# Kernel optimization log

Measured on AMD Instinct MI355X. Metric: run time of the kernel, lower is better.

Reference implementation:

```python
import jax, jax.numpy as jnp
import numpy as np

EMBED_DIM = 1024
NUM_HEADS = 16
HEAD_DIM = EMBED_DIM // NUM_HEADS
ROPE_BASE = 10000.0
SQK_INIT_VALUE = 1.0
SQK_INIT_SCALING = 1.0 / (EMBED_DIM ** 0.5)


def setup_inputs() -> dict:
    key = jax.random.key(0)
    ks = jax.random.split(key, 6)
    B, N = 1, 2048
    x = jax.random.normal(ks[0], (B, N, EMBED_DIM), dtype=jnp.float32)
    # torch nn.Linear weights are [out_features, in_features]; y = x @ W.T
    s = EMBED_DIM ** -0.5
    Wq = jax.random.normal(ks[1], (EMBED_DIM, EMBED_DIM), dtype=jnp.float32) * s
    Wk = jax.random.normal(ks[2], (EMBED_DIM, EMBED_DIM), dtype=jnp.float32) * s
    Wv = jax.random.normal(ks[3], (EMBED_DIM, EMBED_DIM), dtype=jnp.float32) * s
    Wo = jax.random.normal(ks[4], (EMBED_DIM, EMBED_DIM), dtype=jnp.float32) * s
    sqk = SQK_INIT_SCALING * jnp.ones((EMBED_DIM,), dtype=jnp.float32) \
        + 0.01 * jax.random.normal(ks[5], (EMBED_DIM,), dtype=jnp.float32)
    return {"x": x, "Wq": Wq, "Wk": Wk, "Wv": Wv, "Wo": Wo, "sqk": sqk}


def _rope(t, offset=0):
    # t: [b, h, n, d]; rotary position embedding (Lrpe type 1), half-split layout
    d = t.shape[-1]
    n = t.shape[-2]
    inv_freq = 1.0 / (ROPE_BASE ** (jnp.arange(0, d, 2, dtype=jnp.float32) / d))  # [d/2]
    pos = jnp.arange(n, dtype=jnp.float32) + offset                               # [n]
    freqs = pos[:, None] * inv_freq[None, :]                                      # [n, d/2]
    cos = jnp.cos(freqs)
    sin = jnp.sin(freqs)
    t1, t2 = jnp.split(t, 2, axis=-1)
    return jnp.concatenate([t1 * cos - t2 * sin, t1 * sin + t2 * cos], axis=-1)


def _justnorm(t):
    return t / jnp.linalg.norm(t, axis=-1, keepdims=True)


def reference(x, Wq, Wk, Wv, Wo, sqk):
    B, N, E = x.shape
    H, D = NUM_HEADS, HEAD_DIM
    q = jnp.einsum('bne,fe->bnf', x, Wq).reshape(B, N, H, D).transpose(0, 2, 1, 3)
    k = jnp.einsum('bne,fe->bnf', x, Wk).reshape(B, N, H, D).transpose(0, 2, 1, 3)
    v = jnp.einsum('bne,fe->bnf', x, Wv).reshape(B, N, H, D).transpose(0, 2, 1, 3)
    q = _rope(q)
    k = _rope(k)
    # sqk * (init_value / init_scaling), reshaped to (h, 1, d)
    sqk_s = (sqk * (SQK_INIT_VALUE / SQK_INIT_SCALING)).reshape(H, 1, D)
    q = sqk_s * _justnorm(q)
    k = sqk_s * _justnorm(k)
    # SDPA with scale = sqrt(head_dim) (as in the source), causal
    scale = D ** 0.5
    scores = jnp.einsum('bhnd,bhmd->bhnm', q, k) * scale
    causal = jnp.tril(jnp.ones((N, N), dtype=bool))
    scores = jnp.where(causal, scores, -jnp.inf)
    attn = jax.nn.softmax(scores, axis=-1)
    out = jnp.einsum('bhnm,bhmd->bhnd', attn, v)           # [b,h,n,d]
    out = out.transpose(0, 2, 1, 3).reshape(B, N, E)       # [b,n,e]
    out = jnp.einsum('bne,fe->bnf', out, Wo)
    return out
```

## Files before the change

### kernel.cpp

```cpp
#include <hip/hip_runtime.h>
#include <hip/hip_bf16.h>

typedef float f32x4 __attribute__((ext_vector_type(4)));
typedef __bf16 bf16x8 __attribute__((ext_vector_type(8)));
typedef __bf16 bf16x4 __attribute__((ext_vector_type(4)));

__device__ __forceinline__ void gload_lds16(const __bf16* g, __bf16* l) {
  __builtin_amdgcn_global_load_lds(
      (const __attribute__((address_space(1))) void*)g,
      (__attribute__((address_space(3))) void*)l, 16, 0, 0);
}

__global__ __launch_bounds__(256) void convert_all(
    const float* __restrict__ x, const float* __restrict__ wq,
    const float* __restrict__ wk, const float* __restrict__ wv,
    const float* __restrict__ wo, __bf16* __restrict__ dst)
{
  int t = blockIdx.x * 256 + threadIdx.x;
  const float* src; size_t soff;
  if (t < 262144) { src = x; soff = (size_t)t * 8; }
  else {
    int r = (t - 262144) >> 17;
    src = (r == 0) ? wq : (r == 1) ? wk : (r == 2) ? wv : wo;
    soff = (size_t)((t - 262144) & 131071) * 8;
  }
  float4 f0 = *(const float4*)(src + soff);
  float4 f1 = *(const float4*)(src + soff + 4);
  bf16x8 o;
  o[0]=(__bf16)f0.x; o[1]=(__bf16)f0.y; o[2]=(__bf16)f0.z; o[3]=(__bf16)f0.w;
  o[4]=(__bf16)f1.x; o[5]=(__bf16)f1.y; o[6]=(__bf16)f1.z; o[7]=(__bf16)f1.w;
  *(bf16x8*)(dst + (size_t)t * 8) = o;
}

template <int BM, int BN, int BK, typename OutT, bool ROPE>
__global__ __launch_bounds__(256) void gemm_bt(
    const __bf16* __restrict__ A,
    const __bf16* __restrict__ B0, const __bf16* __restrict__ B1, const __bf16* __restrict__ B2,
    OutT* __restrict__ C0, OutT* __restrict__ C1, OutT* __restrict__ C2,
    int M, int N, int K, const float* __restrict__ sqkp)
{
  const __bf16* B = (blockIdx.z == 0) ? B0 : (blockIdx.z == 1) ? B1 : B2;
  OutT* C = (blockIdx.z == 0) ? C0 : (blockIdx.z == 1) ? C1 : C2;

  constexpr int MT = BM / 32, NT = BN / 32, KK = BK / 32;
  constexpr int CPR = BK / 8;
  constexpr int RPI = 64 / CPR;
  __shared__ __align__(16) __bf16 As[BM * BK];
  __shared__ __align__(16) __bf16 Bs[BN * BK];

  const int tid = threadIdx.x, w = tid >> 6, l = tid & 63;
  const int wr = w >> 1, wc = w & 1;
  const int g = l >> 4, c16 = l & 15;
  const int bm = blockIdx.y, bn = blockIdx.x;
  const int lr = l / CPR, lc = l % CPR;

  f32x4 acc[MT][NT] = {};
  const int nk = K / BK;

  for (int kt = 0; kt < nk; ++kt) {
    __syncthreads();
#pragma unroll
    for (int i = w; i < BM / RPI; i += 4) {
      int row = i * RPI + lr;
      int sch = lc ^ (row & 7);
      gload_lds16(A + (size_t)(bm * BM + row) * K + kt * BK + sch * 8, As + i * RPI * BK);
    }
#pragma unroll
    for (int i = w; i < BN / RPI; i += 4) {
      int row = i * RPI + lr;
      int sch = lc ^ (row & 7);
      gload_lds16(B + (size_t)(bn * BN + row) * K + kt * BK + sch * 8, Bs + i * RPI * BK);
    }
    __syncthreads();

#pragma unroll
    for (int kk = 0; kk < KK; ++kk) {
      bf16x8 af[MT], bf[NT];
#pragma unroll
      for (int mt = 0; mt < MT; ++mt) {
        int row = wr * (BM / 2) + mt * 16 + c16;
        af[mt] = *(const bf16x8*)(As + row * BK + (((kk * 4 + g) ^ (row & 7)) * 8));
      }
#pragma unroll
      for (int nt = 0; nt < NT; ++nt) {
        int row = wc * (BN / 2) + nt * 16 + c16;
        bf[nt] = *(const bf16x8*)(Bs + row * BK + (((kk * 4 + g) ^ (row & 7)) * 8));
      }
#pragma unroll
      for (int mt = 0; mt < MT; ++mt)
#pragma unroll
        for (int nt = 0; nt < NT; ++nt)
          acc[mt][nt] = __builtin_amdgcn_mfma_f32_16x16x32_bf16(af[mt], bf[nt], acc[mt][nt], 0, 0, 0);
    }
  }

  bool done = false;
  if constexpr (ROPE) {
    static_assert(!ROPE || NT == 4, "ROPE epilogue assumes BN=128");
    if (blockIdx.z < 2) {
      const bool isQ = (blockIdx.z == 0);
      const int hcol = bn * BN + wc * (BN / 2);
      float sq[4];
#pragma unroll
      for (int nt = 0; nt < 4; ++nt) sq[nt] = sqkp[hcol + nt * 16 + c16] * 32.0f;
      const float QSC = 8.0f * 1.4426950408889634f;
      const float L = 0.415241011860919f;
      const float inv0 = exp2f(-(float)c16 * L);
      const float inv1 = exp2f(-(float)(c16 + 16) * L);
#pragma unroll
      for (int mt = 0; mt < MT; ++mt) {
#pragma unroll
        for (int r = 0; r < 4; ++r) {
          int row = bm * BM + wr * (BM / 2) + mt * 16 + g * 4 + r;
          float s0, c0, s1, c1;
          sincosf((float)row * inv0, &s0, &c0);
          sincosf((float)row * inv1, &s1, &c1);
          float v0 = acc[mt][0][r], v1 = acc[mt][1][r];
          float v2 = acc[mt][2][r], v3 = acc[mt][3][r];
          float n0 = v0 * c0 - v2 * s0;
          float n2 = v0 * s0 + v2 * c0;
          float n1 = v1 * c1 - v3 * s1;
          float n3 = v1 * s1 + v3 * c1;
          float ss = n0 * n0 + n1 * n1 + n2 * n2 + n3 * n3;
#pragma unroll
          for (int m2 = 1; m2 < 16; m2 <<= 1) ss += __shfl_xor(ss, m2, 16);
          float rinv = rsqrtf(ss);
          if (isQ) rinv *= QSC;
          C[(size_t)row * N + hcol +  0 + c16] = (OutT)(n0 * sq[0] * rinv);
          C[(size_t)row * N + hcol + 16 + c16] = (OutT)(n1 * sq[1] * rinv);
          C[(size_t)row * N + hcol + 32 + c16] = (OutT)(n2 * sq[2] * rinv);
          C[(size_t)row * N + hcol + 48 + c16] = (OutT)(n3 * sq[3] * rinv);
        }
      }
      done = true;
    }
  }
  if (!done) {
#pragma unroll
    for (int mt = 0; mt < MT; ++mt)
#pragma unroll
      for (int nt = 0; nt < NT; ++nt)
#pragma unroll
        for (int r = 0; r < 4; ++r) {
          int row = bm * BM + wr * (BM / 2) + mt * 16 + g * 4 + r;
          int col = bn * BN + wc * (BN / 2) + nt * 16 + c16;
          C[(size_t)row * N + col] = (OutT)acc[mt][nt][r];
        }
  }
}

__global__ __launch_bounds__(256) void vtrans(const __bf16* __restrict__ v, __bf16* __restrict__ vt)
{
  __shared__ __align__(16) __bf16 t[64 * 72];
  int h = blockIdx.y;
  int n0 = blockIdx.x * 64;
  int tid = threadIdx.x;
#pragma unroll
  for (int j = 0; j < 2; ++j) {
    int idx = tid + j * 256;
    int r = idx >> 3, c = (idx & 7) * 8;
    bf16x8 val = *(const bf16x8*)(v + (size_t)(n0 + r) * 1024 + h * 64 + c);
    *(bf16x8*)&t[r * 72 + c] = val;
  }
  __syncthreads();
#pragma unroll
  for (int j = 0; j < 2; ++j) {
    int idx = tid + j * 256;
    int d = idx >> 3, nn = (idx & 7) * 8;
    bf16x8 o;
#pragma unroll
    for (int jj = 0; jj < 8; ++jj) o[jj] = t[(nn + jj) * 72 + d];
    *(bf16x8*)(vt + (size_t)(h * 64 + d) * 2048 + n0 + nn) = o;
  }
}

#define STAGE(BUF, KT)                                                         \
  {                                                                            \
    _Pragma("unroll")                                                          \
    for (int p = 0; p < 2; ++p) {                                              \
      int row = srow + p * 32;                                                 \
      int sch = sc ^ (row & 7);                                                \
      gload_lds16(Kg + (size_t)((KT) * 64 + row) * 1024 + h * 64 + sch * 8,    \
                  &Ks[BUF][w * 512 + p * 2048]);                               \
      gload_lds16(Vg + ((size_t)h * 64 + row) * 2048 + (KT) * 64 + sch * 8,    \
                  &Vs[BUF][w * 512 + p * 2048]);                               \
    }                                                                          \
  }

__global__ __launch_bounds__(256, 4) void attn_kernel(
    const __bf16* __restrict__ Qg, const __bf16* __restrict__ Kg,
    const __bf16* __restrict__ Vg, __bf16* __restrict__ Og,
    float* __restrict__ oS, float* __restrict__ lS)
{
  __shared__ __align__(16) __bf16 Ks[2][4096];
  __shared__ __align__(16) __bf16 Vs[2][4096];
  __shared__ __align__(16) __bf16 Ps[4][16 * 72];

  const int b = blockIdx.x;
  int h, qt, kts, kte, sidx;
  if (b < 512) {
    int p = b >> 5;
    qt = 16 + p;
    sidx = (b >> 4) & 1;
    h = b & 15;
    int mid = (qt + 1) >> 1;
    kts = sidx ? mid : 0;
    kte = sidx ? qt : (mid - 1);
  } else {
    qt = 15 - ((b - 512) >> 4);
    h = b & 15;
    kts = 0; kte = qt; sidx = -1;
  }
  const int q0 = qt * 64;

  const int tid = threadIdx.x, w = tid >> 6, l = tid & 63;
  const int g = l >> 4, c16 = l & 15;
  const int srow = tid >> 3;
  const int sc   = tid & 7;

  __bf16* Ps_w = &Ps[w][0];
  const int qig = q0 + w * 16 + c16;

  const __bf16* qbase = Qg + (size_t)qig * 1024 + h * 64 + g * 8;
  const bf16x8 qf0 = *(const bf16x8*)(qbase);
  const bf16x8 qf1 = *(const bf16x8*)(qbase + 32);

  f32x4 o[4] = {};
  float lsum = 0.f;

  STAGE(0, kts)

  for (int kt = kts; kt <= kte; ++kt) {
    const int cur = (kt - kts) & 1;
    __syncthreads();
    if (kt < kte) STAGE(cur ^ 1, kt + 1)

    const __bf16* Kb = Ks[cur];
    const __bf16* Vb = Vs[cur];

    f32x4 s[4] = {};
#pragma unroll
    for (int kjb = 0; kjb < 4; ++kjb) {
      int r = kjb * 16 + c16;
      bf16x8 k0 = *(const bf16x8*)((char*)Kb + r * 128 + ((g ^ (r & 7)) * 16));
      bf16x8 k1 = *(const bf16x8*)((char*)Kb + r * 128 + (((4 + g) ^ (r & 7)) * 16));
      s[kjb] = __builtin_amdgcn_mfma_f32_16x16x32_bf16(k0, qf0, s[kjb], 0, 0, 0);
      s[kjb] = __builtin_amdgcn_mfma_f32_16x16x32_bf16(k1, qf1, s[kjb], 0, 0, 0);
    }

    const bool diag = (kt == qt);
#pragma unroll
    for (int kjb = 0; kjb < 4; ++kjb) {
      bf16x4 pk;
#pragma unroll
      for (int r = 0; r < 4; ++r) {
        float sv = s[kjb][r];
        int kvg = kt * 64 + kjb * 16 + g * 4 + r;
        if (diag && kvg > qig) sv = -1e30f;
        float e = exp2f(sv);
        pk[r] = (__bf16)e;
        lsum += e;
      }
      *(bf16x4*)((char*)Ps_w + c16 * 144 + kjb * 32 + g * 8) = pk;
    }

#pragma unroll
    for (int ks = 0; ks < 2; ++ks) {
      bf16x8 pa = *(const bf16x8*)((char*)Ps_w + c16 * 144 + ks * 64 + g * 16);
#pragma unroll
      for (int nt = 0; nt < 4; ++nt) {
        int r = nt * 16 + c16;
        bf16x8 vb = *(const bf16x8*)((char*)Vb + r * 128 + (((ks * 4 + g) ^ (r & 7)) * 16));
        o[nt] = __builtin_amdgcn_mfma_f32_16x16x32_bf16(pa, vb, o[nt], 0, 0, 0);
      }
    }
  }

  lsum += __shfl_xor(lsum, 16);
  lsum += __shfl_xor(lsum, 32);

  if (sidx < 0) {
    float* lsh = (float*)Ps_w;
    if (g == 0) lsh[c16] = lsum;
    __builtin_amdgcn_s_waitcnt(0);
#pragma unroll
    for (int r = 0; r < 4; ++r) {
      float rinv = 1.0f / lsh[g * 4 + r];
      int qi = q0 + w * 16 + g * 4 + r;
#pragma unroll
      for (int nt = 0; nt < 4; ++nt)
        Og[(size_t)qi * 1024 + h * 64 + nt * 16 + c16] = (__bf16)(o[nt][r] * rinv);
    }
  } else {
    float* oBase = oS + (size_t)sidx * 1024 * 1024;
#pragma unroll
    for (int r = 0; r < 4; ++r) {
      int row = q0 + w * 16 + g * 4 + r - 1024;
#pragma unroll
      for (int nt = 0; nt < 4; ++nt)
        oBase[(size_t)row * 1024 + h * 64 + nt * 16 + c16] = o[nt][r];
    }
    if (g == 0)
      lS[(size_t)sidx * 1024 * 16 + (size_t)(qig - 1024) * 16 + h] = lsum;
  }
}

__global__ __launch_bounds__(256) void merge_halves(
    const float* __restrict__ oS, const float* __restrict__ lS,
    __bf16* __restrict__ Og)
{
  int row = blockIdx.x;
  int col = threadIdx.x * 4;
  int h = col >> 6;
  float lsum = lS[(size_t)row * 16 + h] + lS[(size_t)(1024 + row) * 16 + h];
  float rinv = 1.0f / lsum;
  f32x4 a = *(const f32x4*)(oS + (size_t)row * 1024 + col);
  f32x4 bb = *(const f32x4*)(oS + (size_t)(1024 * 1024) + (size_t)row * 1024 + col);
  f32x4 sum = a + bb;
  bf16x4 ob;
  ob[0] = (__bf16)(sum[0] * rinv); ob[1] = (__bf16)(sum[1] * rinv);
  ob[2] = (__bf16)(sum[2] * rinv); ob[3] = (__bf16)(sum[3] * rinv);
  *(bf16x4*)(Og + (size_t)(1024 + row) * 1024 + col) = ob;
}

extern "C" void kernel_launch(void* const* d_in, const int* in_sizes, int n_in,
                              void* d_out, int out_size, void* d_ws, size_t ws_size,
                              hipStream_t stream) {
  const float* x   = (const float*)d_in[0];
  const float* Wq  = (const float*)d_in[1];
  const float* Wk  = (const float*)d_in[2];
  const float* Wv  = (const float*)d_in[3];
  const float* Wo  = (const float*)d_in[4];
  const float* sqk = (const float*)d_in[5];
  float* out = (float*)d_out;

  __bf16* xb  = (__bf16*)d_ws;
  __bf16* wqb = xb  + (size_t)2048 * 1024;
  __bf16* wkb = wqb + (size_t)1024 * 1024;
  __bf16* wvb = wkb + (size_t)1024 * 1024;
  __bf16* wob = wvb + (size_t)1024 * 1024;
  __bf16* qn  = wob + (size_t)1024 * 1024;
  __bf16* kn  = qn  + (size_t)2048 * 1024;
  __bf16* v   = kn  + (size_t)2048 * 1024;
  __bf16* vtb = v   + (size_t)2048 * 1024;
  __bf16* og  = vtb + (size_t)2048 * 1024;
  float*  oS  = (float*)(og + (size_t)2048 * 1024);
  float*  lS  = oS + (size_t)2 * 1024 * 1024;

  convert_all<<<3072, 256, 0, stream>>>(x, Wq, Wk, Wv, Wo, xb);
  gemm_bt<64, 128, 128, __bf16, true><<<dim3(8, 32, 3), 256, 0, stream>>>(
      xb, wqb, wkb, wvb, qn, kn, v, 2048, 1024, 1024, sqk);
  vtrans<<<dim3(32, 16), 256, 0, stream>>>(v, vtb);
  attn_kernel<<<768, 256, 0, stream>>>(qn, kn, vtb, og, oS, lS);
  merge_halves<<<1024, 256, 0, stream>>>(oS, lS, og);
  gemm_bt<64, 64, 128, float, false><<<dim3(16, 32, 1), 256, 0, stream>>>(
      og, wob, wob, wob, out, out, out, 2048, 1024, 1024, nullptr);
}
```

Baseline: 77.22 us.

## Compute softmax row sums with MFMA, swizzle P tile, add setprio, shrink GEMM K-tile

The attention kernel drops the per-lane scalar accumulation of exp values and the cross-lane shuffle reduction. Instead it gets the row sums from an extra MFMA of P against a vector of ones, so the denominator lands directly in the output row layout. The P staging buffer moves from padded rows to an XOR-swizzled unpadded layout to avoid LDS bank conflicts. s_setprio is raised around the MFMA sections to favour matrix issue across waves. Separately, the K tile of both GEMM launches is halved from 128 to 64, which changes LDS use and occupancy at the cost of more loop iterations.

```diff
diff --git a/kernel.cpp b/kernel.cpp
--- a/kernel.cpp
+++ b/kernel.cpp
@@ -194,7 +194,7 @@
 {
   __shared__ __align__(16) __bf16 Ks[2][4096];
   __shared__ __align__(16) __bf16 Vs[2][4096];
-  __shared__ __align__(16) __bf16 Ps[4][16 * 72];
+  __shared__ __align__(16) __bf16 Ps[4][1024];
 
   const int b = blockIdx.x;
   int h, qt, kts, kte, sidx;
@@ -217,6 +217,7 @@
   const int g = l >> 4, c16 = l & 15;
   const int srow = tid >> 3;
   const int sc   = tid & 7;
+  const int swz  = (c16 & 7) << 4;
 
   __bf16* Ps_w = &Ps[w][0];
   const int qig = q0 + w * 16 + c16;
@@ -225,8 +226,12 @@
   const bf16x8 qf0 = *(const bf16x8*)(qbase);
   const bf16x8 qf1 = *(const bf16x8*)(qbase + 32);
 
+  bf16x8 onesf;
+#pragma unroll
+  for (int j = 0; j < 8; ++j) onesf[j] = (__bf16)1.0f;
+
   f32x4 o[4] = {};
-  float lsum = 0.f;
+  f32x4 ol = {};
 
   STAGE(0, kts)
 
@@ -238,6 +243,7 @@
     const __bf16* Kb = Ks[cur];
     const __bf16* Vb = Vs[cur];
 
+    __builtin_amdgcn_s_setprio(1);
     f32x4 s[4] = {};
 #pragma unroll
     for (int kjb = 0; kjb < 4; ++kjb) {
@@ -247,6 +253,7 @@
       s[kjb] = __builtin_amdgcn_mfma_f32_16x16x32_bf16(k0, qf0, s[kjb], 0, 0, 0);
       s[kjb] = __builtin_amdgcn_mfma_f32_16x16x32_bf16(k1, qf1, s[kjb], 0, 0, 0);
     }
+    __builtin_amdgcn_s_setprio(0);
 
     const bool diag = (kt == qt);
 #pragma unroll
@@ -257,35 +264,32 @@
         float sv = s[kjb][r];
         int kvg = kt * 64 + kjb * 16 + g * 4 + r;
         if (diag && kvg > qig) sv = -1e30f;
-        float e = exp2f(sv);
-        pk[r] = (__bf16)e;
-        lsum += e;
-      }
-      *(bf16x4*)((char*)Ps_w + c16 * 144 + kjb * 32 + g * 8) = pk;
-    }
-
+        pk[r] = (__bf16)exp2f(sv);
+      }
+      int pbyte = (c16 * 128 + kjb * 32 + g * 8) ^ swz;
+      *(bf16x4*)((char*)Ps_w + pbyte) = pk;
+    }
+
+    __builtin_amdgcn_s_setprio(1);
 #pragma unroll
     for (int ks = 0; ks < 2; ++ks) {
-      bf16x8 pa = *(const bf16x8*)((char*)Ps_w + c16 * 144 + ks * 64 + g * 16);
+      int abyte = (c16 * 128 + ks * 64 + g * 16) ^ swz;
+      bf16x8 pa = *(const bf16x8*)((char*)Ps_w + abyte);
 #pragma unroll
       for (int nt = 0; nt < 4; ++nt) {
         int r = nt * 16 + c16;
         bf16x8 vb = *(const bf16x8*)((char*)Vb + r * 128 + (((ks * 4 + g) ^ (r & 7)) * 16));
         o[nt] = __builtin_amdgcn_mfma_f32_16x16x32_bf16(pa, vb, o[nt], 0, 0, 0);
       }
-    }
-  }
-
-  lsum += __shfl_xor(lsum, 16);
-  lsum += __shfl_xor(lsum, 32);
+      ol = __builtin_amdgcn_mfma_f32_16x16x32_bf16(pa, onesf, ol, 0, 0, 0);
+    }
+    __builtin_amdgcn_s_setprio(0);
+  }
 
   if (sidx < 0) {
-    float* lsh = (float*)Ps_w;
-    if (g == 0) lsh[c16] = lsum;
-    __builtin_amdgcn_s_waitcnt(0);
 #pragma unroll
     for (int r = 0; r < 4; ++r) {
-      float rinv = 1.0f / lsh[g * 4 + r];
+      float rinv = 1.0f / ol[r];
       int qi = q0 + w * 16 + g * 4 + r;
 #pragma unroll
       for (int nt = 0; nt < 4; ++nt)
@@ -299,9 +303,9 @@
 #pragma unroll
       for (int nt = 0; nt < 4; ++nt)
         oBase[(size_t)row * 1024 + h * 64 + nt * 16 + c16] = o[nt][r];
-    }
-    if (g == 0)
-      lS[(size_t)sidx * 1024 * 16 + (size_t)(qig - 1024) * 16 + h] = lsum;
+      if (c16 == 0)
+        lS[(size_t)sidx * 1024 * 16 + (size_t)row * 16 + h] = ol[r];
+    }
   }
 }
 
@@ -348,11 +352,11 @@
   float*  lS  = oS + (size_t)2 * 1024 * 1024;
 
   convert_all<<<3072, 256, 0, stream>>>(x, Wq, Wk, Wv, Wo, xb);
-  gemm_bt<64, 128, 128, __bf16, true><<<dim3(8, 32, 3), 256, 0, stream>>>(
+  gemm_bt<64, 128, 64, __bf16, true><<<dim3(8, 32, 3), 256, 0, stream>>>(
       xb, wqb, wkb, wvb, qn, kn, v, 2048, 1024, 1024, sqk);
   vtrans<<<dim3(32, 16), 256, 0, stream>>>(v, vtb);
   attn_kernel<<<768, 256, 0, stream>>>(qn, kn, vtb, og, oS, lS);
   merge_halves<<<1024, 256, 0, stream>>>(oS, lS, og);
-  gemm_bt<64, 64, 128, float, false><<<dim3(16, 32, 1), 256, 0, stream>>>(
+  gemm_bt<64, 64, 64, float, false><<<dim3(16, 32, 1), 256, 0, stream>>>(
       og, wob, wob, wob, out, out, out, 2048, 1024, 1024, nullptr);
 }
```

Result: no change. 77.98 us (+1.0%).
